# Kernel tuning notes

Measured on AMD Instinct MI355X. Metric: run time of the kernel, lower is better.

## Reference

```python
import jax, jax.numpy as jnp
import numpy as np

N, D, W, S = 16384, 256, 64, 8  # utterances, embed dim, attention half-window, speakers


def setup_inputs() -> dict:
    key = jax.random.key(0)
    ks = jax.random.split(key, 8)
    scale = 1.0 / np.sqrt(D)
    return {
        "x": jax.random.normal(ks[0], (N, D), jnp.float32),
        "speaker_ids": jax.random.randint(ks[1], (N,), 0, S, jnp.int32),
        "W_att": jax.random.normal(ks[2], (D, D), jnp.float32) * scale,
        "W_pred": jax.random.normal(ks[3], (D, D), jnp.float32) * scale,
        "W_suc": jax.random.normal(ks[4], (D, D), jnp.float32) * scale,
        "W_same": jax.random.normal(ks[5], (D, D), jnp.float32) * scale,
        "W_diff": jax.random.normal(ks[6], (D, D), jnp.float32) * scale,
    }


def reference(x, speaker_ids, W_att, W_pred, W_suc, W_same, W_diff):
    n = x.shape[0]
    pad = jnp.zeros((W, D), x.dtype)
    # windowed gather: for utterance i, neighbors at offsets [-W, W-1] (2W slots)
    win_idx = jnp.arange(n)[:, None] + jnp.arange(2 * W)[None, :]  # index into padded [N+2W]
    xp = jnp.concatenate([pad, x, pad], axis=0)                    # [N+2W, D]
    windows = xp[win_idx]                                          # [N, 2W, D]
    # raw_attn[i,w] = (edge_att_weights(windows[i,w])) . x[i]
    raw_attn = jnp.einsum("nwd,ed,ne->nw", windows, W_att, x)      # [N, 2W]
    attn = jax.nn.softmax(raw_attn, axis=1)
    # relation masks over the band: j = i + offset
    offs = jnp.arange(2 * W) - W                                   # [-W, W-1]
    j = jnp.arange(n)[:, None] + offs[None, :]                     # [N, 2W]
    valid = (j >= 0) & (j < n)
    jc = jnp.clip(j, 0, n - 1)
    same_spk = speaker_ids[jc] == speaker_ids[:, None]
    masks = [
        valid & (offs >= 0)[None, :],   # pred: edges to current/future within window
        valid & (offs < 0)[None, :],    # suc: edges to past within window
        valid & same_spk,               # same speaker within window
        valid & ~same_spk,              # different speaker within window
    ]
    # relation-specific GCN aggregation: h = sum_r A_r @ (x @ W_r), A_r banded
    h = jnp.zeros_like(x)
    for Wr, m in zip([W_pred, W_suc, W_same, W_diff], masks):
        support = x @ Wr                                           # [N, D]
        sp = jnp.concatenate([pad, support, pad], axis=0)[win_idx]  # [N, 2W, D]
        h = h + jnp.einsum("nw,nwd->nd", attn * m, sp)
    return jax.nn.log_softmax(h, axis=1)
```

## Files before the change

### kernel.cpp

```cpp
#include <hip/hip_runtime.h>
#include <hip/hip_bf16.h>

typedef unsigned short u16;
typedef unsigned int u32;
typedef __attribute__((ext_vector_type(8))) short short8;
typedef __attribute__((ext_vector_type(4))) float floatx4;

#define NU 16384
#define DIM 256
#define AMS 208

#define XHo 0u
#define XLo 4194304u
#define XRo 8388608u
#define YHo 12582912u
#define YLo 16777216u
#define ST0 20971520u
#define STROW 16512u
#define STMAT 4227072u
#define WH0o 33652736u
#define WL0o 33718272u
#define WRo  33783808u

__device__ __forceinline__ u16 bfh(float v) {
  return (u16)(__float_as_uint(v) >> 16);
}
__device__ __forceinline__ float bup(u16 u) {
  return __uint_as_float(((u32)u) << 16);
}
__device__ __forceinline__ u16 bfrn(float v) {
  u32 u = __float_as_uint(v);
  return (u16)((u + 0x7fffu + ((u >> 16) & 1u)) >> 16);
}

__global__ __launch_bounds__(256) void xprep(const float* __restrict__ x,
                                             u16* __restrict__ ws) {
  int idx = (blockIdx.x * 256 + threadIdx.x) * 8;
  float4 v0 = *(const float4*)(x + idx);
  float4 v1 = *(const float4*)(x + idx + 4);
  float a[8] = {v0.x, v0.y, v0.z, v0.w, v1.x, v1.y, v1.z, v1.w};
  u16 h[8], l[8], r[8];
#pragma unroll
  for (int q = 0; q < 8; ++q) {
    h[q] = bfh(a[q]);
    l[q] = bfh(a[q] - bup(h[q]));
    r[q] = bfrn(a[q]);
  }
  *(uint4*)(ws + XHo + idx) = *(const uint4*)h;
  *(uint4*)(ws + XLo + idx) = *(const uint4*)l;
  *(uint4*)(ws + XRo + idx) = *(const uint4*)r;
}

__global__ __launch_bounds__(256) void wpgz(
    const float* __restrict__ wat, const float* __restrict__ wpr,
    const float* __restrict__ wsu, const float* __restrict__ wsm,
    const float* __restrict__ wdf, u16* __restrict__ ws) {
  const int b = blockIdx.x, t = threadIdx.x;
  if (b < 32) {
    const int s = b & 7, mat = b >> 3, n = t;
    const float* Wa = (mat == 0) ? wat : (mat == 1) ? wpr : (mat == 2) ? wsm : wsu;
    const float* Wb = (mat == 0) ? wat : (mat == 1) ? wsu : (mat == 2) ? wdf : wdf;
    const float c1  = (mat == 0) ? 0.f : (mat == 3) ? 1.f : -1.f;
    u16 hbuf[32], lbuf[32];
#pragma unroll 8
    for (int k = 0; k < 32; ++k) {
      float v = Wa[(s * 32 + k) * 256 + n] + c1 * Wb[(s * 32 + k) * 256 + n];
      if (mat == 0) { hbuf[k] = bfh(v); lbuf[k] = bfh(v - bup(hbuf[k])); }
      else          { hbuf[k] = bfrn(v); }
    }
    u16* dh = ws + ((mat == 0) ? WH0o : (WRo + (size_t)(mat - 1) * 65536))
               + (size_t)s * 8192 + n * 32;
#pragma unroll
    for (int p = 0; p < 4; ++p) *(uint4*)(dh + p * 8) = ((const uint4*)hbuf)[p];
    if (mat == 0) {
      u16* dl = ws + WL0o + (size_t)s * 8192 + n * 32;
#pragma unroll
      for (int p = 0; p < 4; ++p) *(uint4*)(dl + p * 8) = ((const uint4*)lbuf)[p];
    }
  } else {
    int g = (b - 32) * 256 + t;
    int r = g >> 13, rem = g & 8191;
    int d = rem >> 5, p = rem & 31;
    size_t base = ST0 + (size_t)r * STMAT + (size_t)d * STROW;
    size_t off = (p < 16) ? (base + p * 4) : (base + 16448 + (p - 16) * 4);
    *(ushort4*)(ws + off) = make_ushort4(0, 0, 0, 0);
  }
}

__global__ __launch_bounds__(512) void gemmS(u16* __restrict__ ws) {
  __shared__ __align__(16) u16 U[37888];

  const int t = threadIdx.x, path = blockIdx.y, row0 = blockIdx.x * 64;
  const int w = t >> 6, ln = t & 15, quad = (t & 63) >> 4, q8 = quad * 8;
  const int n0 = w * 32;

  if (path == 0) {
#pragma unroll
    for (int cc = 0; cc < 8; ++cc) {
      int idx = t + 512 * cc;
      int buf = idx >> 11, e = idx & 2047;
      int row = e >> 5, c8 = (e & 31) * 8;
      *(uint4*)(U + buf * 16896 + row * 264 + c8) =
          *(const uint4*)(ws + (buf ? XLo : XHo) + (size_t)(row0 + row) * 256 + c8);
    }
    __syncthreads();

    floatx4 acc[4][2];
#pragma unroll
    for (int m = 0; m < 4; ++m)
#pragma unroll
      for (int nt = 0; nt < 2; ++nt) acc[m][nt] = (floatx4){0.f, 0.f, 0.f, 0.f};

    for (int s = 0; s < 8; ++s) {
      short8 ah[4], al[4];
#pragma unroll
      for (int m = 0; m < 4; ++m) {
        ah[m] = *(const short8*)(U + (m * 16 + ln) * 264 + s * 32 + q8);
        al[m] = *(const short8*)(U + 16896 + (m * 16 + ln) * 264 + s * 32 + q8);
      }
      short8 bh[2], bl[2];
#pragma unroll
      for (int nt = 0; nt < 2; ++nt) {
        size_t off = (size_t)s * 8192 + (n0 + nt * 16 + ln) * 32 + q8;
        bh[nt] = *(const short8*)(ws + WH0o + off);
        bl[nt] = *(const short8*)(ws + WL0o + off);
      }
#pragma unroll
      for (int m = 0; m < 4; ++m)
#pragma unroll
        for (int nt = 0; nt < 2; ++nt) {
          acc[m][nt] = __builtin_amdgcn_mfma_f32_16x16x32_bf16(ah[m], bh[nt], acc[m][nt], 0, 0, 0);
          acc[m][nt] = __builtin_amdgcn_mfma_f32_16x16x32_bf16(ah[m], bl[nt], acc[m][nt], 0, 0, 0);
          acc[m][nt] = __builtin_amdgcn_mfma_f32_16x16x32_bf16(al[m], bh[nt], acc[m][nt], 0, 0, 0);
        }
    }
#pragma unroll
    for (int m = 0; m < 4; ++m)
#pragma unroll
      for (int nt = 0; nt < 2; ++nt) {
        int col = n0 + nt * 16 + ln;
#pragma unroll
        for (int r = 0; r < 4; ++r) {
          int row = row0 + m * 16 + quad * 4 + r;
          float y = acc[m][nt][r];
          u16 hh = bfh(y);
          ws[YHo + (size_t)row * 256 + col] = hh;
          ws[YLo + (size_t)row * 256 + col] = bfh(y - bup(hh));
        }
      }
  } else {
#pragma unroll
    for (int cc = 0; cc < 4; ++cc) {
      int idx = t + 512 * cc;
      int row = idx >> 5, c8 = (idx & 31) * 8;
      *(uint4*)(U + row * 264 + c8) =
          *(const uint4*)(ws + XRo + (size_t)(row0 + row) * 256 + c8);
    }
    __syncthreads();

    for (int mat = 0; mat < 3; ++mat) {
      floatx4 acc[4][2];
#pragma unroll
      for (int m = 0; m < 4; ++m)
#pragma unroll
        for (int nt = 0; nt < 2; ++nt) acc[m][nt] = (floatx4){0.f, 0.f, 0.f, 0.f};
      for (int s = 0; s < 8; ++s) {
        short8 ah[4];
#pragma unroll
        for (int m = 0; m < 4; ++m)
          ah[m] = *(const short8*)(U + (m * 16 + ln) * 264 + s * 32 + q8);
        short8 bh[2];
#pragma unroll
        for (int nt = 0; nt < 2; ++nt)
          bh[nt] = *(const short8*)(ws + WRo + (size_t)mat * 65536
                                    + (size_t)s * 8192 + (n0 + nt * 16 + ln) * 32 + q8);
#pragma unroll
        for (int m = 0; m < 4; ++m)
#pragma unroll
          for (int nt = 0; nt < 2; ++nt)
            acc[m][nt] = __builtin_amdgcn_mfma_f32_16x16x32_bf16(ah[m], bh[nt], acc[m][nt], 0, 0, 0);
      }
      __syncthreads();
#pragma unroll
      for (int m = 0; m < 4; ++m)
#pragma unroll
        for (int nt = 0; nt < 2; ++nt) {
          int col = n0 + nt * 16 + ln;
          ushort4 pk = make_ushort4(bfrn(acc[m][nt][0]), bfrn(acc[m][nt][1]),
                                    bfrn(acc[m][nt][2]), bfrn(acc[m][nt][3]));
          *(ushort4*)(U + 16896 + col * 80 + m * 16 + quad * 4) = pk;
        }
      __syncthreads();
      u16* STm = ws + ST0 + (size_t)mat * STMAT;
#pragma unroll
      for (int cc = 0; cc < 4; ++cc) {
        int c = t + 512 * cc;
        int d = c >> 3, part = c & 7;
        *(uint4*)(STm + (size_t)d * STROW + 64 + row0 + part * 8) =
            *(const uint4*)(U + 16896 + d * 80 + part * 8);
      }
    }
  }
}

__global__ __launch_bounds__(512) void fused_attn(
    const u16* __restrict__ ws, const int* __restrict__ spk,
    float* __restrict__ out)
{
  __shared__ __align__(16) u16 stg[12288];
  __shared__ __align__(16) u16 Am[64 * AMS];
  __shared__ int spkw[192];
  __shared__ float prt[64][2], prs[64][2];
  __shared__ float red[64][8];

  const int t    = threadIdx.x;
  const int w    = t >> 6;
  const int ln   = t & 15;
  const int quad = (t & 63) >> 4;
  const int q8   = quad * 8;
  const int i0   = blockIdx.x * 64;
  const int mw   = w & 3;
  const int half = w >> 2;

  if (t < 192) spkw[t] = spk[min(max(i0 - 64 + t, 0), NU - 1)];

  floatx4 accP[6];
#pragma unroll
  for (int cc = 0; cc < 6; ++cc) accP[cc] = (floatx4){0.f, 0.f, 0.f, 0.f};

  for (int kd = 0; kd < DIM; kd += 32) {
#pragma unroll
    for (int cc = 0; cc < 3; ++cc) {
      int idx = t + 512 * cc;
      int buf = (idx >= 768) ? 1 : 0;
      int e   = idx - buf * 768;
      int row = e >> 2, c8 = (e & 3) * 8;
      int jc  = min(max(i0 + row - 64, 0), NU - 1);
      *(uint4*)(stg + buf * 6144 + row * 32 + c8) =
          *(const uint4*)(ws + (buf ? XLo : XHo) + (size_t)jc * 256 + kd + c8);
    }
    __syncthreads();

    size_t yo = (size_t)(i0 + mw * 16 + ln) * 256 + kd + q8;
    short8 yh8 = *(const short8*)(ws + YHo + yo);
    short8 yl8 = *(const short8*)(ws + YLo + yo);
#pragma unroll
    for (int cc = 0; cc < 6; ++cc) {
      int xrow = half * 96 + cc * 16 + ln;
      short8 xbh = *(const short8*)(stg + xrow * 32 + q8);
      short8 xbl = *(const short8*)(stg + 6144 + xrow * 32 + q8);
      accP[cc] = __builtin_amdgcn_mfma_f32_16x16x32_bf16(yh8, xbh, accP[cc], 0, 0, 0);
      accP[cc] = __builtin_amdgcn_mfma_f32_16x16x32_bf16(yh8, xbl, accP[cc], 0, 0, 0);
      accP[cc] = __builtin_amdgcn_mfma_f32_16x16x32_bf16(yl8, xbh, accP[cc], 0, 0, 0);
    }
    __syncthreads();
  }

  int  c_of[6];
  bool vj[6];
#pragma unroll
  for (int cc = 0; cc < 6; ++cc) {
    c_of[cc] = half * 96 + cc * 16 + ln;
    int j = i0 + c_of[cc] - 64;
    vj[cc] = (j >= 0) && (j < NU);
  }
#pragma unroll
  for (int r = 0; r < 4; ++r) {
    int row = mw * 16 + quad * 4 + r;
    float mx = -3.4e38f;
#pragma unroll
    for (int cc = 0; cc < 6; ++cc) {
      int rel = c_of[cc] - row;
      bool inb = (rel >= 0) && (rel < 128);
      if (inb) mx = fmaxf(mx, vj[cc] ? accP[cc][r] : 0.f);
    }
#pragma unroll
    for (int o = 1; o < 16; o <<= 1) mx = fmaxf(mx, __shfl_xor(mx, o));
    if (ln == 0) prt[row][half] = mx;
  }
  __syncthreads();
#pragma unroll
  for (int r = 0; r < 4; ++r) {
    int row = mw * 16 + quad * 4 + r;
    float gm = fmaxf(prt[row][0], prt[row][1]);
    float s = 0.f;
#pragma unroll
    for (int cc = 0; cc < 6; ++cc) {
      int rel = c_of[cc] - row;
      bool inb = (rel >= 0) && (rel < 128);
      float vv = vj[cc] ? accP[cc][r] : 0.f;
      float e  = inb ? __expf(vv - gm) : 0.f;
      s += e;
      accP[cc][r] = (inb && vj[cc]) ? e : 0.f;
    }
#pragma unroll
    for (int o = 1; o < 16; o <<= 1) s += __shfl_xor(s, o);
    if (ln == 0) prs[row][half] = s;
  }
  __syncthreads();
#pragma unroll
  for (int r = 0; r < 4; ++r) {
    int row = mw * 16 + quad * 4 + r;
    float inv = 1.f / (prs[row][0] + prs[row][1]);
#pragma unroll
    for (int cc = 0; cc < 6; ++cc)
      Am[row * AMS + c_of[cc]] = bfrn(accP[cc][r] * inv);
  }
  __syncthreads();

  const int n0 = w * 32;
  floatx4 acc2[4][2];
#pragma unroll
  for (int m = 0; m < 4; ++m)
#pragma unroll
    for (int nt = 0; nt < 2; ++nt) acc2[m][nt] = (floatx4){0.f, 0.f, 0.f, 0.f};

  const int arow = t >> 3, aseg = t & 7;
  const int sr = spkw[arow + 64];

  for (int kj = 0; kj < 192; kj += 32) {
    {
      u16 b0[4], b1[4], b2[4];
#pragma unroll
      for (int q = 0; q < 4; ++q) {
        int c = kj + aseg * 4 + q;
        u16 a = Am[arow * AMS + c];
        b0[q] = (c - arow >= 64) ? a : (u16)0;
        b1[q] = (spkw[c] == sr) ? a : (u16)0;
        b2[q] = a;
      }
      *(ushort4*)(stg + (0 * 64 + arow) * 32 + aseg * 4) = *(const ushort4*)b0;
      *(ushort4*)(stg + (2048 + arow * 32) + aseg * 4)   = *(const ushort4*)b1;
      *(ushort4*)(stg + (4096 + arow * 32) + aseg * 4)   = *(const ushort4*)b2;
    }
    __syncthreads();

#pragma unroll
    for (int rel = 0; rel < 3; ++rel) {
      short8 af[4];
#pragma unroll
      for (int m = 0; m < 4; ++m)
        af[m] = *(const short8*)(stg + rel * 2048 + (m * 16 + ln) * 32 + q8);
#pragma unroll
      for (int nt = 0; nt < 2; ++nt) {
        size_t so = (size_t)ST0 + (size_t)rel * STMAT
                  + (size_t)(n0 + nt * 16 + ln) * STROW + (i0 + kj) + q8;
        short8 bf8 = *(const short8*)(ws + so);
#pragma unroll
        for (int m = 0; m < 4; ++m)
          acc2[m][nt] = __builtin_amdgcn_mfma_f32_16x16x32_bf16(af[m], bf8, acc2[m][nt], 0, 0, 0);
      }
    }
    __syncthreads();
  }

#pragma unroll
  for (int m = 0; m < 4; ++m)
#pragma unroll
    for (int r = 0; r < 4; ++r) {
      float v = fmaxf(acc2[m][0][r], acc2[m][1][r]);
#pragma unroll
      for (int o = 1; o < 16; o <<= 1) v = fmaxf(v, __shfl_xor(v, o));
      if (ln == 0) red[m * 16 + quad * 4 + r][w] = v;
    }
  __syncthreads();
  float gmx[4][4];
#pragma unroll
  for (int m = 0; m < 4; ++m)
#pragma unroll
    for (int r = 0; r < 4; ++r) {
      int row = m * 16 + quad * 4 + r;
      float g = red[row][0];
#pragma unroll
      for (int ww = 1; ww < 8; ++ww) g = fmaxf(g, red[row][ww]);
      gmx[m][r] = g;
    }
  __syncthreads();
#pragma unroll
  for (int m = 0; m < 4; ++m)
#pragma unroll
    for (int r = 0; r < 4; ++r) {
      float e = __expf(acc2[m][0][r] - gmx[m][r]) + __expf(acc2[m][1][r] - gmx[m][r]);
#pragma unroll
      for (int o = 1; o < 16; o <<= 1) e += __shfl_xor(e, o);
      if (ln == 0) red[m * 16 + quad * 4 + r][w] = e;
    }
  __syncthreads();
#pragma unroll
  for (int m = 0; m < 4; ++m)
#pragma unroll
    for (int r = 0; r < 4; ++r) {
      int row = m * 16 + quad * 4 + r;
      float s = red[row][0];
#pragma unroll
      for (int ww = 1; ww < 8; ++ww) s += red[row][ww];
      float lse = gmx[m][r] + logf(s);
      size_t rowg = (size_t)(i0 + row) * DIM;
      out[rowg + n0 + ln]      = acc2[m][0][r] - lse;
      out[rowg + n0 + 16 + ln] = acc2[m][1][r] - lse;
    }
}

extern "C" void kernel_launch(void* const* d_in, const int* in_sizes, int n_in,
                              void* d_out, int out_size, void* d_ws, size_t ws_size,
                              hipStream_t stream) {
  const float* x   = (const float*)d_in[0];
  const int*   spk = (const int*)d_in[1];
  const float* wat = (const float*)d_in[2];
  const float* wpr = (const float*)d_in[3];
  const float* wsu = (const float*)d_in[4];
  const float* wsm = (const float*)d_in[5];
  const float* wdf = (const float*)d_in[6];
  float* out = (float*)d_out;
  u16* ws = (u16*)d_ws;

  hipLaunchKernelGGL(xprep, dim3(2048), dim3(256), 0, stream, x, ws);
  hipLaunchKernelGGL(wpgz, dim3(128), dim3(256), 0, stream,
                     wat, wpr, wsu, wsm, wdf, ws);
  hipLaunchKernelGGL(gemmS, dim3(256, 2), dim3(512), 0, stream, ws);
  hipLaunchKernelGGL(fused_attn, dim3(256), dim3(512), 0, stream, ws, spk, out);
}
```

Measured before the change: 156.2 us.

## Merge prep kernels, drop separate rounded x copy, double fused_attn block width

The two preprocessing kernels become one launch. The hi/lo bf16 split now uses round-to-nearest, so the hi part can also stand in for the rounded x copy, which removes one 8MB workspace array and its write and read. fused_attn now runs 1024 threads per block instead of 512, with each wave covering fewer columns, to add parallelism within the 256 blocks. The larger block adds extra staging branches and a wider cross-wave reduction, and may lower registers available per thread.

```diff
diff --git a/kernel.cpp b/kernel.cpp
--- a/kernel.cpp
+++ b/kernel.cpp
@@ -9,22 +9,19 @@
 #define NU 16384
 #define DIM 256
 #define AMS 208
+#define XST 264
 
 #define XHo 0u
 #define XLo 4194304u
-#define XRo 8388608u
-#define YHo 12582912u
-#define YLo 16777216u
-#define ST0 20971520u
+#define YHo 8388608u
+#define YLo 12582912u
+#define ST0 16777216u
 #define STROW 16512u
 #define STMAT 4227072u
-#define WH0o 33652736u
-#define WL0o 33718272u
-#define WRo  33783808u
-
-__device__ __forceinline__ u16 bfh(float v) {
-  return (u16)(__float_as_uint(v) >> 16);
-}
+#define WH0o 29458432u
+#define WL0o 29523968u
+#define WRo  29589504u
+
 __device__ __forceinline__ float bup(u16 u) {
   return __uint_as_float(((u32)u) << 16);
 }
@@ -33,52 +30,52 @@
   return (u16)((u + 0x7fffu + ((u >> 16) & 1u)) >> 16);
 }
 
-__global__ __launch_bounds__(256) void xprep(const float* __restrict__ x,
-                                             u16* __restrict__ ws) {
-  int idx = (blockIdx.x * 256 + threadIdx.x) * 8;
-  float4 v0 = *(const float4*)(x + idx);
-  float4 v1 = *(const float4*)(x + idx + 4);
-  float a[8] = {v0.x, v0.y, v0.z, v0.w, v1.x, v1.y, v1.z, v1.w};
-  u16 h[8], l[8], r[8];
-#pragma unroll
-  for (int q = 0; q < 8; ++q) {
-    h[q] = bfh(a[q]);
-    l[q] = bfh(a[q] - bup(h[q]));
-    r[q] = bfrn(a[q]);
-  }
-  *(uint4*)(ws + XHo + idx) = *(const uint4*)h;
-  *(uint4*)(ws + XLo + idx) = *(const uint4*)l;
-  *(uint4*)(ws + XRo + idx) = *(const uint4*)r;
-}
-
-__global__ __launch_bounds__(256) void wpgz(
+__global__ __launch_bounds__(256) void prep(
+    const float* __restrict__ x,
     const float* __restrict__ wat, const float* __restrict__ wpr,
     const float* __restrict__ wsu, const float* __restrict__ wsm,
     const float* __restrict__ wdf, u16* __restrict__ ws) {
   const int b = blockIdx.x, t = threadIdx.x;
-  if (b < 32) {
-    const int s = b & 7, mat = b >> 3, n = t;
+  if (b < 2048) {
+    int idx = (b * 256 + t) * 8;
+    float4 v0 = *(const float4*)(x + idx);
+    float4 v1 = *(const float4*)(x + idx + 4);
+    float a[8] = {v0.x, v0.y, v0.z, v0.w, v1.x, v1.y, v1.z, v1.w};
+    u16 h[8], l[8];
+#pragma unroll
+    for (int q = 0; q < 8; ++q) {
+      h[q] = bfrn(a[q]);
+      l[q] = bfrn(a[q] - bup(h[q]));
+    }
+    *(uint4*)(ws + XHo + idx) = *(const uint4*)h;
+    *(uint4*)(ws + XLo + idx) = *(const uint4*)l;
+  } else if (b < 2064) {
+    const int bp = b - 2048;
+    const int mat = bp >> 2, n = t;
     const float* Wa = (mat == 0) ? wat : (mat == 1) ? wpr : (mat == 2) ? wsm : wsu;
     const float* Wb = (mat == 0) ? wat : (mat == 1) ? wsu : (mat == 2) ? wdf : wdf;
     const float c1  = (mat == 0) ? 0.f : (mat == 3) ? 1.f : -1.f;
-    u16 hbuf[32], lbuf[32];
+    for (int si = 0; si < 2; ++si) {
+      const int s = (bp & 3) * 2 + si;
+      u16 hbuf[32], lbuf[32];
 #pragma unroll 8
-    for (int k = 0; k < 32; ++k) {
-      float v = Wa[(s * 32 + k) * 256 + n] + c1 * Wb[(s * 32 + k) * 256 + n];
-      if (mat == 0) { hbuf[k] = bfh(v); lbuf[k] = bfh(v - bup(hbuf[k])); }
-      else          { hbuf[k] = bfrn(v); }
-    }
-    u16* dh = ws + ((mat == 0) ? WH0o : (WRo + (size_t)(mat - 1) * 65536))
-               + (size_t)s * 8192 + n * 32;
-#pragma unroll
-    for (int p = 0; p < 4; ++p) *(uint4*)(dh + p * 8) = ((const uint4*)hbuf)[p];
-    if (mat == 0) {
-      u16* dl = ws + WL0o + (size_t)s * 8192 + n * 32;
-#pragma unroll
-      for (int p = 0; p < 4; ++p) *(uint4*)(dl + p * 8) = ((const uint4*)lbuf)[p];
+      for (int k = 0; k < 32; ++k) {
+        float v = Wa[(s * 32 + k) * 256 + n] + c1 * Wb[(s * 32 + k) * 256 + n];
+        hbuf[k] = bfrn(v);
+        if (mat == 0) lbuf[k] = bfrn(v - bup(hbuf[k]));
+      }
+      u16* dh = ws + ((mat == 0) ? WH0o : (WRo + (size_t)(mat - 1) * 65536))
+                 + (size_t)s * 8192 + n * 32;
+#pragma unroll
+      for (int p = 0; p < 4; ++p) *(uint4*)(dh + p * 8) = ((const uint4*)hbuf)[p];
+      if (mat == 0) {
+        u16* dl = ws + WL0o + (size_t)s * 8192 + n * 32;
+#pragma unroll
+        for (int p = 0; p < 4; ++p) *(uint4*)(dl + p * 8) = ((const uint4*)lbuf)[p];
+      }
     }
   } else {
-    int g = (b - 32) * 256 + t;
+    int g = (b - 2064) * 256 + t;
     int r = g >> 13, rem = g & 8191;
     int d = rem >> 5, p = rem & 31;
     size_t base = ST0 + (size_t)r * STMAT + (size_t)d * STROW;
@@ -100,7 +97,7 @@
       int idx = t + 512 * cc;
       int buf = idx >> 11, e = idx & 2047;
       int row = e >> 5, c8 = (e & 31) * 8;
-      *(uint4*)(U + buf * 16896 + row * 264 + c8) =
+      *(uint4*)(U + buf * 16896 + row * XST + c8) =
           *(const uint4*)(ws + (buf ? XLo : XHo) + (size_t)(row0 + row) * 256 + c8);
     }
     __syncthreads();
@@ -115,8 +112,8 @@
       short8 ah[4], al[4];
 #pragma unroll
       for (int m = 0; m < 4; ++m) {
-        ah[m] = *(const short8*)(U + (m * 16 + ln) * 264 + s * 32 + q8);
-        al[m] = *(const short8*)(U + 16896 + (m * 16 + ln) * 264 + s * 32 + q8);
+        ah[m] = *(const short8*)(U + (m * 16 + ln) * XST + s * 32 + q8);
+        al[m] = *(const short8*)(U + 16896 + (m * 16 + ln) * XST + s * 32 + q8);
       }
       short8 bh[2], bl[2];
 #pragma unroll
@@ -143,9 +140,9 @@
         for (int r = 0; r < 4; ++r) {
           int row = row0 + m * 16 + quad * 4 + r;
           float y = acc[m][nt][r];
-          u16 hh = bfh(y);
+          u16 hh = bfrn(y);
           ws[YHo + (size_t)row * 256 + col] = hh;
-          ws[YLo + (size_t)row * 256 + col] = bfh(y - bup(hh));
+          ws[YLo + (size_t)row * 256 + col] = bfrn(y - bup(hh));
         }
       }
   } else {
@@ -153,8 +150,8 @@
     for (int cc = 0; cc < 4; ++cc) {
       int idx = t + 512 * cc;
       int row = idx >> 5, c8 = (idx & 31) * 8;
-      *(uint4*)(U + row * 264 + c8) =
-          *(const uint4*)(ws + XRo + (size_t)(row0 + row) * 256 + c8);
+      *(uint4*)(U + row * XST + c8) =
+          *(const uint4*)(ws + XHo + (size_t)(row0 + row) * 256 + c8);
     }
     __syncthreads();
 
@@ -168,7 +165,7 @@
         short8 ah[4];
 #pragma unroll
         for (int m = 0; m < 4; ++m)
-          ah[m] = *(const short8*)(U + (m * 16 + ln) * 264 + s * 32 + q8);
+          ah[m] = *(const short8*)(U + (m * 16 + ln) * XST + s * 32 + q8);
         short8 bh[2];
 #pragma unroll
         for (int nt = 0; nt < 2; ++nt)
@@ -203,15 +200,15 @@
   }
 }
 
-__global__ __launch_bounds__(512) void fused_attn(
+__global__ __launch_bounds__(1024) void fused_attn(
     const u16* __restrict__ ws, const int* __restrict__ spk,
     float* __restrict__ out)
 {
-  __shared__ __align__(16) u16 stg[12288];
+  __shared__ __align__(16) u16 B_[12288];
   __shared__ __align__(16) u16 Am[64 * AMS];
   __shared__ int spkw[192];
-  __shared__ float prt[64][2], prs[64][2];
-  __shared__ float red[64][8];
+  __shared__ float prt[64][4], prs[64][4];
+  __shared__ float red[64][16];
 
   const int t    = threadIdx.x;
   const int w    = t >> 6;
@@ -220,24 +217,31 @@
   const int q8   = quad * 8;
   const int i0   = blockIdx.x * 64;
   const int mw   = w & 3;
-  const int half = w >> 2;
+  const int cg   = w >> 2;
 
   if (t < 192) spkw[t] = spk[min(max(i0 - 64 + t, 0), NU - 1)];
 
-  floatx4 accP[6];
-#pragma unroll
-  for (int cc = 0; cc < 6; ++cc) accP[cc] = (floatx4){0.f, 0.f, 0.f, 0.f};
+  floatx4 accP[3];
+#pragma unroll
+  for (int cc = 0; cc < 3; ++cc) accP[cc] = (floatx4){0.f, 0.f, 0.f, 0.f};
 
   for (int kd = 0; kd < DIM; kd += 32) {
-#pragma unroll
-    for (int cc = 0; cc < 3; ++cc) {
-      int idx = t + 512 * cc;
+    {
+      int idx = t;
       int buf = (idx >= 768) ? 1 : 0;
       int e   = idx - buf * 768;
       int row = e >> 2, c8 = (e & 3) * 8;
       int jc  = min(max(i0 + row - 64, 0), NU - 1);
-      *(uint4*)(stg + buf * 6144 + row * 32 + c8) =
+      *(uint4*)(B_ + buf * 6144 + row * 32 + c8) =
           *(const uint4*)(ws + (buf ? XLo : XHo) + (size_t)jc * 256 + kd + c8);
+      if (t < 512) {
+        idx = t + 1024;
+        e   = idx - 768;
+        row = e >> 2; c8 = (e & 3) * 8;
+        jc  = min(max(i0 + row - 64, 0), NU - 1);
+        *(uint4*)(B_ + 6144 + row * 32 + c8) =
+            *(const uint4*)(ws + XLo + (size_t)jc * 256 + kd + c8);
+      }
     }
     __syncthreads();
 
@@ -245,10 +249,10 @@
     short8 yh8 = *(const short8*)(ws + YHo + yo);
     short8 yl8 = *(const short8*)(ws + YLo + yo);
 #pragma unroll
-    for (int cc = 0; cc < 6; ++cc) {
-      int xrow = half * 96 + cc * 16 + ln;
-      short8 xbh = *(const short8*)(stg + xrow * 32 + q8);
-      short8 xbl = *(const short8*)(stg + 6144 + xrow * 32 + q8);
+    for (int cc = 0; cc < 3; ++cc) {
+      int xrow = (cg * 3 + cc) * 16 + ln;
+      short8 xbh = *(const short8*)(B_ + xrow * 32 + q8);
+      short8 xbl = *(const short8*)(B_ + 6144 + xrow * 32 + q8);
       accP[cc] = __builtin_amdgcn_mfma_f32_16x16x32_bf16(yh8, xbh, accP[cc], 0, 0, 0);
       accP[cc] = __builtin_amdgcn_mfma_f32_16x16x32_bf16(yh8, xbl, accP[cc], 0, 0, 0);
       accP[cc] = __builtin_amdgcn_mfma_f32_16x16x32_bf16(yl8, xbh, accP[cc], 0, 0, 0);
@@ -256,11 +260,11 @@
     __syncthreads();
   }
 
-  int  c_of[6];
-  bool vj[6];
-#pragma unroll
-  for (int cc = 0; cc < 6; ++cc) {
-    c_of[cc] = half * 96 + cc * 16 + ln;
+  int  c_of[3];
+  bool vj[3];
+#pragma unroll
+  for (int cc = 0; cc < 3; ++cc) {
+    c_of[cc] = (cg * 3 + cc) * 16 + ln;
     int j = i0 + c_of[cc] - 64;
     vj[cc] = (j >= 0) && (j < NU);
   }
@@ -269,23 +273,24 @@
     int row = mw * 16 + quad * 4 + r;
     float mx = -3.4e38f;
 #pragma unroll
-    for (int cc = 0; cc < 6; ++cc) {
+    for (int cc = 0; cc < 3; ++cc) {
       int rel = c_of[cc] - row;
       bool inb = (rel >= 0) && (rel < 128);
       if (inb) mx = fmaxf(mx, vj[cc] ? accP[cc][r] : 0.f);
     }
 #pragma unroll
     for (int o = 1; o < 16; o <<= 1) mx = fmaxf(mx, __shfl_xor(mx, o));
-    if (ln == 0) prt[row][half] = mx;
+    if (ln == 0) prt[row][cg] = mx;
   }
   __syncthreads();
 #pragma unroll
   for (int r = 0; r < 4; ++r) {
     int row = mw * 16 + quad * 4 + r;
-    float gm = fmaxf(prt[row][0], prt[row][1]);
+    float gm = fmaxf(fmaxf(prt[row][0], prt[row][1]),
+                     fmaxf(prt[row][2], prt[row][3]));
     float s = 0.f;
 #pragma unroll
-    for (int cc = 0; cc < 6; ++cc) {
+    for (int cc = 0; cc < 3; ++cc) {
       int rel = c_of[cc] - row;
       bool inb = (rel >= 0) && (rel < 128);
       float vv = vj[cc] ? accP[cc][r] : 0.f;
@@ -295,31 +300,29 @@
     }
 #pragma unroll
     for (int o = 1; o < 16; o <<= 1) s += __shfl_xor(s, o);
-    if (ln == 0) prs[row][half] = s;
+    if (ln == 0) prs[row][cg] = s;
   }
   __syncthreads();
 #pragma unroll
   for (int r = 0; r < 4; ++r) {
     int row = mw * 16 + quad * 4 + r;
-    float inv = 1.f / (prs[row][0] + prs[row][1]);
-#pragma unroll
-    for (int cc = 0; cc < 6; ++cc)
+    float inv = 1.f / (prs[row][0] + prs[row][1] + prs[row][2] + prs[row][3]);
+#pragma unroll
+    for (int cc = 0; cc < 3; ++cc)
       Am[row * AMS + c_of[cc]] = bfrn(accP[cc][r] * inv);
   }
   __syncthreads();
 
-  const int n0 = w * 32;
-  floatx4 acc2[4][2];
-#pragma unroll
-  for (int m = 0; m < 4; ++m)
-#pragma unroll
-    for (int nt = 0; nt < 2; ++nt) acc2[m][nt] = (floatx4){0.f, 0.f, 0.f, 0.f};
+  const int n0 = w * 16;
+  floatx4 acc2[4];
+#pragma unroll
+  for (int m = 0; m < 4; ++m) acc2[m] = (floatx4){0.f, 0.f, 0.f, 0.f};
 
   const int arow = t >> 3, aseg = t & 7;
-  const int sr = spkw[arow + 64];
+  const int sr = (t < 512) ? spkw[arow + 64] : 0;
 
   for (int kj = 0; kj < 192; kj += 32) {
-    {
+    if (t < 512) {
       u16 b0[4], b1[4], b2[4];
 #pragma unroll
       for (int q = 0; q < 4; ++q) {
@@ -329,9 +332,9 @@
         b1[q] = (spkw[c] == sr) ? a : (u16)0;
         b2[q] = a;
       }
-      *(ushort4*)(stg + (0 * 64 + arow) * 32 + aseg * 4) = *(const ushort4*)b0;
-      *(ushort4*)(stg + (2048 + arow * 32) + aseg * 4)   = *(const ushort4*)b1;
-      *(ushort4*)(stg + (4096 + arow * 32) + aseg * 4)   = *(const ushort4*)b2;
+      *(ushort4*)(B_ + (0 * 64 + arow) * 32 + aseg * 4) = *(const ushort4*)b0;
+      *(ushort4*)(B_ + (2048 + arow * 32) + aseg * 4)   = *(const ushort4*)b1;
+      *(ushort4*)(B_ + (4096 + arow * 32) + aseg * 4)   = *(const ushort4*)b2;
     }
     __syncthreads();
 
@@ -340,16 +343,13 @@
       short8 af[4];
 #pragma unroll
       for (int m = 0; m < 4; ++m)
-        af[m] = *(const short8*)(stg + rel * 2048 + (m * 16 + ln) * 32 + q8);
-#pragma unroll
-      for (int nt = 0; nt < 2; ++nt) {
-        size_t so = (size_t)ST0 + (size_t)rel * STMAT
-                  + (size_t)(n0 + nt * 16 + ln) * STROW + (i0 + kj) + q8;
-        short8 bf8 = *(const short8*)(ws + so);
-#pragma unroll
-        for (int m = 0; m < 4; ++m)
-          acc2[m][nt] = __builtin_amdgcn_mfma_f32_16x16x32_bf16(af[m], bf8, acc2[m][nt], 0, 0, 0);
-      }
+        af[m] = *(const short8*)(B_ + rel * 2048 + (m * 16 + ln) * 32 + q8);
+      size_t so = (size_t)ST0 + (size_t)rel * STMAT
+                + (size_t)(n0 + ln) * STROW + (i0 + kj) + q8;
+      short8 bf8 = *(const short8*)(ws + so);
+#pragma unroll
+      for (int m = 0; m < 4; ++m)
+        acc2[m] = __builtin_amdgcn_mfma_f32_16x16x32_bf16(af[m], bf8, acc2[m], 0, 0, 0);
     }
     __syncthreads();
   }
@@ -358,7 +358,7 @@
   for (int m = 0; m < 4; ++m)
 #pragma unroll
     for (int r = 0; r < 4; ++r) {
-      float v = fmaxf(acc2[m][0][r], acc2[m][1][r]);
+      float v = acc2[m][r];
 #pragma unroll
       for (int o = 1; o < 16; o <<= 1) v = fmaxf(v, __shfl_xor(v, o));
       if (ln == 0) red[m * 16 + quad * 4 + r][w] = v;
@@ -372,7 +372,7 @@
       int row = m * 16 + quad * 4 + r;
       float g = red[row][0];
 #pragma unroll
-      for (int ww = 1; ww < 8; ++ww) g = fmaxf(g, red[row][ww]);
+      for (int ww = 1; ww < 16; ++ww) g = fmaxf(g, red[row][ww]);
       gmx[m][r] = g;
     }
   __syncthreads();
@@ -380,7 +380,7 @@
   for (int m = 0; m < 4; ++m)
 #pragma unroll
     for (int r = 0; r < 4; ++r) {
-      float e = __expf(acc2[m][0][r] - gmx[m][r]) + __expf(acc2[m][1][r] - gmx[m][r]);
+      float e = __expf(acc2[m][r] - gmx[m][r]);
 #pragma unroll
       for (int o = 1; o < 16; o <<= 1) e += __shfl_xor(e, o);
       if (ln == 0) red[m * 16 + quad * 4 + r][w] = e;
@@ -393,11 +393,9 @@
       int row = m * 16 + quad * 4 + r;
       float s = red[row][0];
 #pragma unroll
-      for (int ww = 1; ww < 8; ++ww) s += red[row][ww];
+      for (int ww = 1; ww < 16; ++ww) s += red[row][ww];
       float lse = gmx[m][r] + logf(s);
-      size_t rowg = (size_t)(i0 + row) * DIM;
-      out[rowg + n0 + ln]      = acc2[m][0][r] - lse;
-      out[rowg + n0 + 16 + ln] = acc2[m][1][r] - lse;
+      out[(size_t)(i0 + row) * DIM + n0 + ln] = acc2[m][r] - lse;
     }
 }
 
@@ -414,9 +412,8 @@
   float* out = (float*)d_out;
   u16* ws = (u16*)d_ws;
 
-  hipLaunchKernelGGL(xprep, dim3(2048), dim3(256), 0, stream, x, ws);
-  hipLaunchKernelGGL(wpgz, dim3(128), dim3(256), 0, stream,
-                     wat, wpr, wsu, wsm, wdf, ws);
+  hipLaunchKernelGGL(prep, dim3(2160), dim3(256), 0, stream,
+                     x, wat, wpr, wsu, wsm, wdf, ws);
   hipLaunchKernelGGL(gemmS, dim3(256, 2), dim3(512), 0, stream, ws);
-  hipLaunchKernelGGL(fused_attn, dim3(256), dim3(512), 0, stream, ws, spk, out);
-}
+  hipLaunchKernelGGL(fused_attn, dim3(256), dim3(1024), 0, stream, ws, spk, out);
+}
```

Result: slower. 190.8 us (+22.2%).
